# Performance work log

Hardware: AMD Instinct MI355X
Metric: run time of the kernel (lower is better)

## Reference

```python
import jax, jax.numpy as jnp
import numpy as np

NH = 12      # attention heads
EPS = 1e-5   # torch nn.LayerNorm default


def _ln(x, g, b):
    m = jnp.mean(x, axis=-1, keepdims=True)
    v = jnp.var(x, axis=-1, keepdims=True)
    return (x - m) * jax.lax.rsqrt(v + EPS) * g + b


def _rel_table(table, n):
    # q_size == k_size == n, table length == 2n-1 -> pure gather, no interpolation
    idx = jnp.arange(n)[:, None] - jnp.arange(n)[None, :] + (n - 1)
    return table[idx]  # (n, n, head_dim)


def _attn2d(x, qkv_w, qkv_b, proj_w, proj_b, rel_h, rel_w):
    B, H, W, C = x.shape
    hd = C // NH
    scale = hd ** -0.5
    N = H * W
    qkv = x.reshape(B, N, C) @ qkv_w + qkv_b                    # (B, N, 3C)
    qkv = qkv.reshape(B, N, 3, NH, hd).transpose(2, 0, 3, 1, 4).reshape(3, B * NH, N, hd)
    q, k, v = qkv[0], qkv[1], qkv[2]
    attn = jnp.einsum('bnd,bmd->bnm', q * scale, k)             # (B*NH, N, N)
    Rh = _rel_table(rel_h, H)
    Rw = _rel_table(rel_w, W)
    rq = q.reshape(B * NH, H, W, hd)                            # unscaled q, as in torch
    bias_h = jnp.einsum('bhwc,hkc->bhwk', rq, Rh)
    bias_w = jnp.einsum('bhwc,wkc->bhwk', rq, Rw)
    attn = (attn.reshape(B * NH, H, W, H, W)
            + bias_h[:, :, :, :, None]
            + bias_w[:, :, :, None, :]).reshape(B * NH, N, N)
    attn = jax.nn.softmax(attn, axis=-1)
    out = (attn @ v).reshape(B, NH, H, W, hd).transpose(0, 2, 3, 1, 4).reshape(B, H, W, C)
    return out @ proj_w + proj_b


def _win_part(x, ws):
    B, H, W, C = x.shape
    ph = (ws - H % ws) % ws
    pw = (ws - W % ws) % ws
    x = jnp.pad(x, ((0, 0), (0, ph), (0, pw), (0, 0)))
    Hp, Wp = H + ph, W + pw
    x = x.reshape(B, Hp // ws, ws, Wp // ws, ws, C).transpose(0, 1, 3, 2, 4, 5)
    return x.reshape(-1, ws, ws, C), (Hp, Wp)


def _win_unpart(wins, ws, pad_hw, hw):
    Hp, Wp = pad_hw
    H, W = hw
    B = wins.shape[0] // (Hp * Wp // ws // ws)
    x = wins.reshape(B, Hp // ws, Wp // ws, ws, ws, -1).transpose(0, 1, 3, 2, 4, 5)
    x = x.reshape(B, Hp, Wp, -1)
    return x[:, :H, :W, :]


def _block(x, ws, ln1g, ln1b, qkvw, qkvb, projw, projb, relh, relw,
           ln2g, ln2b, mw1, mb1, mw2, mb2):
    shortcut = x
    x = _ln(x, ln1g, ln1b)
    if ws > 0:
        H, W = x.shape[1], x.shape[2]
        x, pad_hw = _win_part(x, ws)
    x = _attn2d(x, qkvw, qkvb, projw, projb, relh, relw)
    if ws > 0:
        x = _win_unpart(x, ws, pad_hw, (H, W))
    x = shortcut + x
    h = _ln(x, ln2g, ln2b)
    h = jax.nn.gelu(h @ mw1 + mb1, approximate=False) @ mw2 + mb2
    return x + h


def setup_inputs() -> dict:
    key = jax.random.key(0)
    def rnd(i, shape, s=0.02):
        return jax.random.normal(jax.random.fold_in(key, i), shape, jnp.float32) * s
    C, M, HD = 768, 3072, 64
    d = {
        'x': rnd(0, (1, 3, 1024, 1024), 1.0),
        'patch_w': rnd(1, (16, 16, 3, C)),
        'patch_b': rnd(2, (C,)),
        'pos_embed': rnd(3, (1, 64, 64, C)),
    }
    i = 4
    for s, L in (('1', 27), ('2', 127)):
        for name, shape in (('ln1g', (C,)), ('ln1b', (C,)), ('qkvw', (C, 3 * C)),
                            ('qkvb', (3 * C,)), ('projw', (C, C)), ('projb', (C,)),
                            ('relh', (L, HD)), ('relw', (L, HD)),
                            ('ln2g', (C,)), ('ln2b', (C,)),
                            ('mw1', (C, M)), ('mb1', (M,)), ('mw2', (M, C)), ('mb2', (C,))):
            d[name + s] = rnd(i, shape)
            i += 1
    for s in ('1', '2'):
        d['ln1g' + s] = d['ln1g' + s] + 1.0
        d['ln2g' + s] = d['ln2g' + s] + 1.0
    return d


def reference(x, patch_w, patch_b, pos_embed,
              ln1g1, ln1b1, qkvw1, qkvb1, projw1, projb1, relh1, relw1,
              ln2g1, ln2b1, mw11, mb11, mw21, mb21,
              ln1g2, ln1b2, qkvw2, qkvb2, projw2, projb2, relh2, relw2,
              ln2g2, ln2b2, mw12, mb12, mw22, mb22):
    # patch embed: 16x16 stride-16 conv, output NHWC (B, 64, 64, 768)
    feat = jax.lax.conv_general_dilated(
        x, patch_w, window_strides=(16, 16), padding='VALID',
        dimension_numbers=('NCHW', 'HWIO', 'NHWC'))
    feat = feat + patch_b + pos_embed
    feat = _block(feat, 14, ln1g1, ln1b1, qkvw1, qkvb1, projw1, projb1,
                  relh1, relw1, ln2g1, ln2b1, mw11, mb11, mw21, mb21)
    feat = _block(feat, 0, ln1g2, ln1b2, qkvw2, qkvb2, projw2, projb2,
                  relh2, relw2, ln2g2, ln2b2, mw12, mb12, mw22, mb22)
    return feat
```

## Files before the change

kernel.cpp:

```cpp
#include <hip/hip_runtime.h>


using u16 = unsigned short;
using u32 = unsigned int;
using short8  = __attribute__((ext_vector_type(8))) short;
using floatx4 = __attribute__((ext_vector_type(4))) float;

__device__ __forceinline__ float bfu2f(u16 u) { return __builtin_bit_cast(float, (u32)u << 16); }
__device__ __forceinline__ u16   f2bfu(float f) {
  u32 u = __builtin_bit_cast(u32, f);
  return (u16)((u + 0x7fffu + ((u >> 16) & 1u)) >> 16);
}
__device__ __forceinline__ u32 cvtpk_bf16(float a, float b) {
  u32 r; asm("v_cvt_pk_bf16_f32 %0, %1, %2" : "=v"(r) : "v"(a), "v"(b)); return r;
}
#define DIV14(x) (((x) * 4682) >> 16)
#define WAIT_VM0()   __builtin_amdgcn_s_waitcnt(0x3f70)
#define WAIT_LGKM0() __builtin_amdgcn_s_waitcnt(0xc07f)

__device__ __forceinline__ void gld_lds16(const u16* g, u16* l) {
  __builtin_amdgcn_global_load_lds(
      (const __attribute__((address_space(1))) u32*)g,
      (__attribute__((address_space(3))) u32*)l, 16, 0, 0);
}

__global__ __launch_bounds__(256) void detect_k(const u16* __restrict__ x, int* __restrict__ flag)
{
  __shared__ int tot;
  if (threadIdx.x == 0) tot = 0;
  __syncthreads();
  int cnt = 0;
  for (int i = threadIdx.x; i < 4096; i += 256) {
    int e = (x[2 * i] >> 7) & 0xFF;
    cnt += (e >= 100 && e <= 134) ? 1 : 0;
  }
  atomicAdd(&tot, cnt);
  __syncthreads();
  if (threadIdx.x == 0) *flag = (tot >= 2458) ? 1 : 0;
}

struct CvtEnt { const void* src; int n; int dstoff; };
struct CvtArgs { CvtEnt e[24]; int cnt; };

__global__ __launch_bounds__(256) void tobf_multi_k(CvtArgs a, u16* __restrict__ dst,
                                                    const int* __restrict__ flag)
{
  int gid = blockIdx.x * 256 + threadIdx.x;
  bool isbf = (*flag != 0);
  for (int t = 0; t < a.cnt; ++t)
    if (gid < a.e[t].n)
      dst[a.e[t].dstoff + gid] = isbf ? ((const u16*)a.e[t].src)[gid]
                                      : f2bfu(((const float*)a.e[t].src)[gid]);
}

__global__ __launch_bounds__(256) void tobf4_k(const void* __restrict__ src, u16* __restrict__ dst,
                                               int n4, const int* __restrict__ flag)
{
  int i = blockIdx.x * 256 + threadIdx.x;
  if (i >= n4) return;
  ushort4 o;
  if (*flag) o = ((const ushort4*)src)[i];
  else {
    float4 f = ((const float4*)src)[i];
    o.x = f2bfu(f.x); o.y = f2bfu(f.y); o.z = f2bfu(f.z); o.w = f2bfu(f.w);
  }
  ((ushort4*)dst)[i] = o;
}

struct TJob { const void* src; int dstoff; int K; int N; int blk0; };
struct TArgs { TJob j[6]; int njobs; };

__global__ __launch_bounds__(256) void tobfT_multi_k(TArgs a, u16* __restrict__ wa,
                                                     const int* __restrict__ flag)
{
  __shared__ u16 t[64][65];
  const int bid = blockIdx.x;
  int ji = 0;
  #pragma unroll
  for (int q = 1; q < 6; ++q) if (q < a.njobs && bid >= a.j[q].blk0) ji = q;
  const void* src = a.j[ji].src;
  u16* dst = wa + a.j[ji].dstoff;
  const int K = a.j[ji].K, N = a.j[ji].N;
  const int local = bid - a.j[ji].blk0;
  const int nx = N >> 6;
  const int bx = local % nx, by = local / nx;
  const int n0 = bx * 64, k0 = by * 64;
  const int r = threadIdx.x >> 2, c = (threadIdx.x & 3) * 16;
  if (*flag) {
    const u16* s = (const u16*)src + (size_t)(k0 + r) * N + n0 + c;
    union { uint4 v[2]; u16 e[16]; } u;
    u.v[0] = *(const uint4*)s; u.v[1] = *(const uint4*)(s + 8);
    #pragma unroll
    for (int j = 0; j < 16; ++j) t[c + j][r] = u.e[j];
  } else {
    const float* s = (const float*)src + (size_t)(k0 + r) * N + n0 + c;
    #pragma unroll
    for (int j = 0; j < 16; ++j) t[c + j][r] = f2bfu(s[j]);
  }
  __syncthreads();
  union { uint4 v[2]; u16 e[16]; } o;
  #pragma unroll
  for (int j = 0; j < 16; ++j) o.e[j] = t[r][c + j];
  u16* d = dst + (size_t)(n0 + r) * K + k0 + c;
  *(uint4*)d = o.v[0]; *(uint4*)(d + 8) = o.v[1];
}

__global__ __launch_bounds__(256) void im2col_k(const void* __restrict__ xv, u16* __restrict__ a,
                                                const int* __restrict__ flag)
{
  int t = blockIdx.x, tid = threadIdx.x;
  int py = t >> 6, px = t & 63;
  int ky = tid >> 4, kx = tid & 15;
  size_t src = (size_t)(py * 16 + ky) * 1024 + px * 16 + kx;
  u16 v0, v1, v2;
  if (*flag) {
    const u16* x = (const u16*)xv;
    v0 = x[src]; v1 = x[src + 1048576]; v2 = x[src + 2097152];
  } else {
    const float* x = (const float*)xv;
    v0 = f2bfu(x[src]); v1 = f2bfu(x[src + 1048576]); v2 = f2bfu(x[src + 2097152]);
  }
  size_t dst = (size_t)t * 768 + tid * 3;
  a[dst] = v0; a[dst + 1] = v1; a[dst + 2] = v2;
}

__global__ __launch_bounds__(256) void ln_k(const float* __restrict__ x,
                                            const u16* __restrict__ g,
                                            const u16* __restrict__ b,
                                            u16* __restrict__ y)
{
  const int t = blockIdx.x, tid = threadIdx.x;
  const float* xp = x + (size_t)t * 768;
  float v0 = xp[tid], v1 = xp[tid + 256], v2 = xp[tid + 512];
  float s = v0 + v1 + v2;
  float q = v0 * v0 + v1 * v1 + v2 * v2;
  #pragma unroll
  for (int off = 32; off; off >>= 1) { s += __shfl_xor(s, off); q += __shfl_xor(q, off); }
  __shared__ float red[8];
  int wid = tid >> 6, lane = tid & 63;
  if (lane == 0) { red[wid] = s; red[4 + wid] = q; }
  __syncthreads();
  s = red[0] + red[1] + red[2] + red[3];
  q = red[4] + red[5] + red[6] + red[7];
  float mean = s * (1.f / 768.f);
  float var  = q * (1.f / 768.f) - mean * mean;
  float rstd = rsqrtf(var + 1e-5f);
  u16* yp = y + (size_t)t * 768;
  yp[tid]       = f2bfu((v0 - mean) * rstd * bfu2f(g[tid])       + bfu2f(b[tid]));
  yp[tid + 256] = f2bfu((v1 - mean) * rstd * bfu2f(g[tid + 256]) + bfu2f(b[tid + 256]));
  yp[tid + 512] = f2bfu((v2 - mean) * rstd * bfu2f(g[tid + 512]) + bfu2f(b[tid + 512]));
}

__global__ __launch_bounds__(256) void ln_win_k(const float* __restrict__ x,
                                                const u16* __restrict__ g,
                                                const u16* __restrict__ b,
                                                u16* __restrict__ wout)
{
  const int t = blockIdx.x, tid = threadIdx.x;
  const int win = t / 196, tok = t - win * 196;
  const int ty = DIV14(tok), tx = tok - 14 * ty;
  const int gy = (win / 5) * 14 + ty, gx = (win % 5) * 14 + tx;
  u16* yp = wout + (size_t)t * 768;
  if (gy >= 64 || gx >= 64) {
    yp[tid] = 0; yp[tid + 256] = 0; yp[tid + 512] = 0;
    return;
  }
  const float* xp = x + (size_t)(gy * 64 + gx) * 768;
  float v0 = xp[tid], v1 = xp[tid + 256], v2 = xp[tid + 512];
  float s = v0 + v1 + v2;
  float q = v0 * v0 + v1 * v1 + v2 * v2;
  #pragma unroll
  for (int off = 32; off; off >>= 1) { s += __shfl_xor(s, off); q += __shfl_xor(q, off); }
  __shared__ float red[8];
  int wid = tid >> 6, lane = tid & 63;
  if (lane == 0) { red[wid] = s; red[4 + wid] = q; }
  __syncthreads();
  s = red[0] + red[1] + red[2] + red[3];
  q = red[4] + red[5] + red[6] + red[7];
  float mean = s * (1.f / 768.f);
  float var  = q * (1.f / 768.f) - mean * mean;
  float rstd = rsqrtf(var + 1e-5f);
  yp[tid]       = f2bfu((v0 - mean) * rstd * bfu2f(g[tid])       + bfu2f(b[tid]));
  yp[tid + 256] = f2bfu((v1 - mean) * rstd * bfu2f(g[tid + 256]) + bfu2f(b[tid + 256]));
  yp[tid + 512] = f2bfu((v2 - mean) * rstd * bfu2f(g[tid + 512]) + bfu2f(b[tid + 512]));
}

enum { MODE_FEAT = 0, MODE_QKV = 1, MODE_RES = 2, MODE_GELU = 3, MODE_OUT = 4 };

template<int BN>
__global__ __launch_bounds__(256) void mgemm_k(
    const u16* __restrict__ A, const u16* __restrict__ Bt, const u16* __restrict__ bias,
    int M, int N, int K, int mode,
    float* __restrict__ outf, u16* __restrict__ outb,
    const float* __restrict__ res, const u16* __restrict__ pos,
    u16* __restrict__ qb, u16* __restrict__ kb, u16* __restrict__ vt, int TW,
    const int* __restrict__ flagp)
{
  constexpr int NWN = BN / 64, NWM = 4 / NWN;
  constexpr int WTM = 128 / NWM;
  constexpr int MS = WTM / 16, NS = 4;
  __shared__ __align__(16) u16 As[2][128 * 32];
  __shared__ __align__(16) u16 Bs[2][BN * 32];
  const int tid = threadIdx.x;
  const int wid = tid >> 6, lane = tid & 63;
  const int l15 = lane & 15, quad = lane >> 4;
  const int wm = wid / NWN, wn = wid % NWN;
  const int m0 = blockIdx.y * 128, n0 = blockIdx.x * BN;

  floatx4 acc[MS][NS];
  #pragma unroll
  for (int i = 0; i < MS; ++i)
    #pragma unroll
    for (int j = 0; j < NS; ++j) acc[i][j] = (floatx4){0.f, 0.f, 0.f, 0.f};

  const int sr = lane >> 2, sc = (lane & 3) * 8;
  const u16* ag0 = A + (size_t)min(m0 + wid * 32 + sr,      M - 1) * K + sc;
  const u16* ag1 = A + (size_t)min(m0 + wid * 32 + 16 + sr, M - 1) * K + sc;
  const u16 *bg0 = nullptr, *bg1 = nullptr;
  if constexpr (BN == 128) {
    bg0 = Bt + (size_t)(n0 + wid * 32 + sr) * K + sc;
    bg1 = Bt + (size_t)(n0 + wid * 32 + 16 + sr) * K + sc;
  } else {
    bg0 = Bt + (size_t)(n0 + wid * 16 + sr) * K + sc;
  }

  auto issue = [&](int buf, int k0) {
    gld_lds16(ag0 + k0, &As[buf][(wid * 32) * 32]);
    gld_lds16(ag1 + k0, &As[buf][(wid * 32 + 16) * 32]);
    if constexpr (BN == 128) {
      gld_lds16(bg0 + k0, &Bs[buf][(wid * 32) * 32]);
      gld_lds16(bg1 + k0, &Bs[buf][(wid * 32 + 16) * 32]);
    } else {
      gld_lds16(bg0 + k0, &Bs[buf][(wid * 16) * 32]);
    }
  };

  issue(0, 0);
  int bufi = 0;
  for (int k0 = 0; k0 < K; k0 += 32, bufi ^= 1) {
    WAIT_VM0();
    __syncthreads();
    if (k0 + 32 < K) issue(bufi ^ 1, k0 + 32);
    short8 af[MS], bf[NS];
    #pragma unroll
    for (int ms = 0; ms < MS; ++ms)
      af[ms] = *(const short8*)&As[bufi][(wm * WTM + ms * 16 + l15) * 32 + quad * 8];
    #pragma unroll
    for (int ns = 0; ns < NS; ++ns)
      bf[ns] = *(const short8*)&Bs[bufi][(wn * 64 + ns * 16 + l15) * 32 + quad * 8];
    #pragma unroll
    for (int ms = 0; ms < MS; ++ms)
      #pragma unroll
      for (int ns = 0; ns < NS; ++ns)
        acc[ms][ns] = __builtin_amdgcn_mfma_f32_16x16x32_bf16(af[ms], bf[ns], acc[ms][ns], 0, 0, 0);
  }

  const bool outbf = (mode == MODE_OUT) ? (*flagp != 0) : false;
  #pragma unroll
  for (int ms = 0; ms < MS; ++ms) {
    const int gmb = m0 + wm * WTM + ms * 16 + quad * 4;
    #pragma unroll
    for (int ns = 0; ns < NS; ++ns) {
      const int gn = n0 + wn * 64 + ns * 16 + l15;
      const float bb = bfu2f(bias[gn]);
      if (mode == MODE_QKV) {
        const int s = gn / 768, nn = gn - s * 768, h = nn >> 6, d = nn & 63;
        #pragma unroll
        for (int r = 0; r < 4; ++r) {
          int gm = gmb + r; if (gm >= M) continue;
          float v = acc[ms][ns][r] + bb;
          int b = gm / TW, tok = gm - b * TW;
          size_t bh = (size_t)(b * 12 + h);
          if (s == 0)      qb[(bh * TW + tok) * 64 + d] = f2bfu(v);
          else if (s == 1) kb[(bh * TW + tok) * 64 + d] = f2bfu(v);
          else             vt[(bh * 64 + d) * TW + tok] = f2bfu(v);
        }
      } else {
        #pragma unroll
        for (int r = 0; r < 4; ++r) {
          int gm = gmb + r; if (gm >= M) continue;
          size_t o = (size_t)gm * N + gn;
          float v = acc[ms][ns][r] + bb;
          if (mode == MODE_FEAT)      outf[o] = v + bfu2f(pos[o]);
          else if (mode == MODE_RES)  outf[o] = v + res[o];
          else if (mode == MODE_GELU) outb[o] = f2bfu(0.5f * v * (1.f + erff(v * 0.70710678f)));
          else {
            float ov = v + res[o];
            if (outbf) outb[o] = f2bfu(ov);
            else       outf[o] = ov;
          }
        }
      }
    }
  }
}

template<int NT, int TD, bool WIN>
__global__ __launch_bounds__(256) void flash_k(
    const u16* __restrict__ qb, const u16* __restrict__ kb, const u16* __restrict__ vt,
    const u16* __restrict__ relh, const u16* __restrict__ relw,
    u16* __restrict__ outb)
{
  constexpr int NTAB = 2 * TD - 1;
  constexpr int KT = (NT + 63) >> 6;
  constexpr float L2E = 1.4426950408889634f;
  constexpr float SC2 = 0.125f * L2E;
  constexpr int RQ  = 0;
  constexpr int RK0 = 4096;
  constexpr int RK1 = WIN ? 4096 : 8192;
  constexpr int RV0 = WIN ? 8192 : 12288;
  constexpr int RV1 = WIN ? 8192 : 16384;
  constexpr int RG  = WIN ? 12288 : 20480;
  constexpr int GWWIN = RG + 64 * 34;
  constexpr int TOT = WIN ? (GWWIN + 64 * 34) : (RG + 64 * 66);
  __shared__ __align__(16) u16 lds[TOT];

  const int tid = threadIdx.x, wid = tid >> 6, lane = tid & 63;
  const int l15 = lane & 15, quad = lane >> 4;
  const int qt = blockIdx.x, bh = blockIdx.y;
  const int q0 = qt * 64;
  const size_t kvbase = (size_t)bh * NT * 64;
  const size_t vbase  = (size_t)bh * 64 * NT;
  const int myrow = wid * 16 + l15;

  auto swb = [](int row, int blk) { return row * 64 + (((blk ^ row) & 7) << 3); };

  {
    const int r = tid >> 2, cb = (tid & 3) * 2;
    const int tok = min(q0 + r, NT - 1);
    const uint4* p = (const uint4*)(qb + kvbase + (size_t)tok * 64 + cb * 8);
    *(uint4*)&lds[RQ + swb(r, cb)]     = p[0];
    *(uint4*)&lds[RQ + swb(r, cb + 1)] = p[1];
  }
  __syncthreads();
  short8 qf[2];
  qf[0] = *(const short8*)&lds[RQ + swb(myrow, quad)];
  qf[1] = *(const short8*)&lds[RQ + swb(myrow, 4 + quad)];
  WAIT_LGKM0();

  auto stageRB = [&](const u16* tab, int rowoff, int maxrow) {
    const int r = tid >> 2, cb = (tid & 3) * 2;
    const int tr = min(rowoff + r, maxrow);
    const uint4* p = (const uint4*)(tab + (size_t)tr * 64 + cb * 8);
    *(uint4*)&lds[RV0 + swb(r, cb)]     = p[0];
    *(uint4*)&lds[RV0 + swb(r, cb + 1)] = p[1];
  };
  auto gpass = [&](int gbase, int gstride, int ncols) {
    for (int ns = 0; ns < ncols / 16; ++ns) {
      floatx4 g = (floatx4){0.f, 0.f, 0.f, 0.f};
      #pragma unroll
      for (int ks = 0; ks < 2; ++ks) {
        short8 b = *(const short8*)&lds[RV0 + swb(ns * 16 + l15, ks * 4 + quad)];
        g = __builtin_amdgcn_mfma_f32_16x16x32_bf16(qf[ks], b, g, 0, 0, 0);
      }
      #pragma unroll
      for (int r = 0; r < 4; ++r)
        lds[gbase + (wid * 16 + quad * 4 + r) * gstride + ns * 16 + l15] = f2bfu(g[r] * L2E);
    }
  };

  float gwv[4][4];
  if constexpr (!WIN) {
    stageRB(relh, qt, NTAB - 1);  __syncthreads();
    gpass(RG, 66, 64);
    __syncthreads();
    stageRB(relw, 0, NTAB - 1);   __syncthreads();
    gpass(RK0, 66, 64);
    #pragma unroll
    for (int kbi = 0; kbi < 4; ++kbi)
      #pragma unroll
      for (int r = 0; r < 4; ++r) {
        const int iw = myrow + 63 - (kbi * 16 + quad * 4 + r);
        if (iw < 64) gwv[kbi][r] = bfu2f(lds[RK0 + myrow * 66 + iw]);
      }
    WAIT_LGKM0();
    __syncthreads();
    stageRB(relw, 64, NTAB - 1);  __syncthreads();
    gpass(RK0, 66, 64);
    #pragma unroll
    for (int kbi = 0; kbi < 4; ++kbi)
      #pragma unroll
      for (int r = 0; r < 4; ++r) {
        const int iw = myrow + 63 - (kbi * 16 + quad * 4 + r);
        if (iw >= 64) gwv[kbi][r] = bfu2f(lds[RK0 + myrow * 66 + iw - 64]);
      }
    WAIT_LGKM0();
  } else {
    stageRB(relh, 0, NTAB - 1);  __syncthreads();
    gpass(RG, 34, 32);
    __syncthreads();
    stageRB(relw, 0, NTAB - 1);  __syncthreads();
    gpass(GWWIN, 34, 32);
  }

  const int srow = lane >> 3;
  const int scol = (((lane & 7) ^ srow) & 7) << 3;
  const u16* kp  = kb + kvbase + (size_t)(wid * 16 + srow) * 64 + scol;
  const u16* kp2 = kp + 512;
  const u16* vp  = vt + vbase  + (size_t)(wid * 16 + srow) * NT + scol;
  const u16* vp2 = vp + (size_t)8 * NT;
  u16* const kd0 = &lds[RK0 + wid * 1024];
  u16* const kd1 = &lds[RK1 + wid * 1024];
  u16* const vd0 = &lds[RV0 + wid * 1024];
  u16* const vd1 = &lds[RV1 + wid * 1024];
  auto issueKV = [&](int buf) {
    u16* kdb = buf ? kd1 : kd0;
    u16* vdb = buf ? vd1 : vd0;
    gld_lds16(kp,  kdb);
    gld_lds16(kp2, kdb + 512);
    gld_lds16(vp,  vdb);
    gld_lds16(vp2, vdb + 512);
    kp += 4096; kp2 += 4096; vp += 64; vp2 += 64;
  };

  float mI = -3e38f, lI = 0.f;
  floatx4 Oacc[4];
  #pragma unroll
  for (int d = 0; d < 4; ++d) Oacc[d] = (floatx4){0.f, 0.f, 0.f, 0.f};

  int qy = 0, qx = 0;
  if constexpr (WIN) {
    const int tok0 = q0 + myrow;
    qy = DIV14(tok0); qx = tok0 - 14 * qy;
  }

  auto body = [&](int RKb, int RVb, int kt) {
    floatx4 sacc[4];
    #pragma unroll
    for (int kbi = 0; kbi < 4; ++kbi) sacc[kbi] = (floatx4){0.f, 0.f, 0.f, 0.f};
    __builtin_amdgcn_s_setprio(1);
    #pragma unroll
    for (int ks = 0; ks < 2; ++ks)
      #pragma unroll
      for (int kbi = 0; kbi < 4; ++kbi) {
        short8 a = *(const short8*)&lds[RKb + swb(kbi * 16 + l15, ks * 4 + quad)];
        sacc[kbi] = __builtin_amdgcn_mfma_f32_16x16x32_bf16(a, qf[ks], sacc[kbi], 0, 0, 0);
      }
    __builtin_amdgcn_s_setprio(0);

    float sv[4][4];
    if constexpr (!WIN) {
      #pragma unroll
      for (int kbi = 0; kbi < 4; ++kbi)
        #pragma unroll
        for (int r = 0; r < 4; ++r)
          sv[kbi][r] = fmaf(SC2, sacc[kbi][r], gwv[kbi][r]);
    } else {
      #pragma unroll
      for (int kbi = 0; kbi < 4; ++kbi)
        #pragma unroll
        for (int r = 0; r < 4; ++r) {
          const int j = kt * 64 + kbi * 16 + quad * 4 + r;
          const int ky = DIV14(j), kx = j - 14 * ky;
          int ih = qy - ky + 13; ih = max(0, min(ih, 31));
          int iw = qx - kx + 13; iw = max(0, min(iw, 31));
          float s = SC2 * sacc[kbi][r] + bfu2f(lds[RG + myrow * 34 + ih])
                                       + bfu2f(lds[GWWIN + myrow * 34 + iw]);
          sv[kbi][r] = (j < NT) ? s : -1e30f;
        }
    }

    float rm;
    {
      float a0 = fmaxf(fmaxf(sv[0][0], sv[0][1]), fmaxf(sv[0][2], sv[0][3]));
      float a1 = fmaxf(fmaxf(sv[1][0], sv[1][1]), fmaxf(sv[1][2], sv[1][3]));
      float a2 = fmaxf(fmaxf(sv[2][0], sv[2][1]), fmaxf(sv[2][2], sv[2][3]));
      float a3 = fmaxf(fmaxf(sv[3][0], sv[3][1]), fmaxf(sv[3][2], sv[3][3]));
      rm = fmaxf(fmaxf(a0, a1), fmaxf(a2, a3));
    }
    rm = fmaxf(rm, __shfl_xor(rm, 16));
    rm = fmaxf(rm, __shfl_xor(rm, 32));
    float ghv = 0.f;
    if constexpr (!WIN) ghv = bfu2f(lds[RG + myrow * 66 + (63 - kt)]);
    const float mt = rm + ghv;
    const float mn = fmaxf(mI, mt);
    const float tt = mn - ghv;

    float rs = 0.f;
    u32 pk[8];
    #pragma unroll
    for (int kbi = 0; kbi < 4; ++kbi) {
      float p0 = __builtin_amdgcn_exp2f(sv[kbi][0] - tt);
      float p1 = __builtin_amdgcn_exp2f(sv[kbi][1] - tt);
      float p2 = __builtin_amdgcn_exp2f(sv[kbi][2] - tt);
      float p3 = __builtin_amdgcn_exp2f(sv[kbi][3] - tt);
      rs += (p0 + p1) + (p2 + p3);
      pk[2 * kbi]     = cvtpk_bf16(p0, p1);
      pk[2 * kbi + 1] = cvtpk_bf16(p2, p3);
    }

    #pragma unroll
    for (int kbi = 0; kbi < 4; ++kbi) {
      const int col = kbi * 16 + quad * 4;
      uint2 w2; w2.x = pk[2 * kbi]; w2.y = pk[2 * kbi + 1];
      *(uint2*)&lds[RQ + myrow * 64 + ((((col >> 3) ^ myrow) & 7) << 3) + (col & 7)] = w2;
    }

    const float al = __builtin_amdgcn_exp2f(mI - mn);
    if (__any(mt > mI)) {
      #pragma unroll
      for (int d = 0; d < 4; ++d) Oacc[d] *= al;
    }
    mI = mn;

    __builtin_amdgcn_s_setprio(1);
    #pragma unroll
    for (int ks = 0; ks < 2; ++ks) {
      short8 pb = *(const short8*)&lds[RQ + swb(myrow, ks * 4 + quad)];
      #pragma unroll
      for (int d = 0; d < 4; ++d) {
        short8 a = *(const short8*)&lds[RVb + swb(d * 16 + l15, ks * 4 + quad)];
        Oacc[d] = __builtin_amdgcn_mfma_f32_16x16x32_bf16(a, pb, Oacc[d], 0, 0, 0);
      }
    }
    __builtin_amdgcn_s_setprio(0);

    rs += __shfl_xor(rs, 16);
    rs += __shfl_xor(rs, 32);
    lI = fmaf(lI, al, rs);
  };

  if constexpr (!WIN) {
    __syncthreads();
    issueKV(0);
    for (int kt = 0; kt < KT; kt += 2) {
      WAIT_VM0();
      __syncthreads();
      if (kt + 1 < KT) issueKV(1);
      body(RK0, RV0, kt);
      WAIT_VM0();
      __syncthreads();
      if (kt + 2 < KT) issueKV(0);
      body(RK1, RV1, kt + 1);
    }
  } else {
    for (int kt = 0; kt < KT; ++kt) {
      __syncthreads();
      {
        const int r = tid >> 2, cb = (tid & 3) * 2;
        const int key = min(kt * 64 + r, NT - 1);
        const uint4* p = (const uint4*)(kb + kvbase + (size_t)key * 64 + cb * 8);
        *(uint4*)&lds[RK0 + swb(r, cb)]     = p[0];
        *(uint4*)&lds[RK0 + swb(r, cb + 1)] = p[1];
      }
      {
        const int d = tid >> 2, c = (tid & 3) << 4;
        if (kt * 64 + c + 15 < NT) {
          #pragma unroll
          for (int h = 0; h < 4; ++h) {
            uint2 v = *(const uint2*)(vt + vbase + (size_t)d * NT + kt * 64 + c + h * 4);
            const int col = c + h * 4;
            *(uint2*)&lds[RV0 + d * 64 + ((((col >> 3) ^ d) & 7) << 3) + (col & 7)] = v;
          }
        } else {
          #pragma unroll
          for (int j = 0; j < 16; ++j) {
            int key = min(kt * 64 + c + j, NT - 1);
            const int col = c + j;
            lds[RV0 + d * 64 + ((((col >> 3) ^ d) & 7) << 3) + (col & 7)] =
                vt[vbase + (size_t)d * NT + key];
          }
        }
      }
      __syncthreads();
      body(RK0, RV0, kt);
    }
  }

  const float rinv = 1.f / lI;
  const int tok = q0 + myrow;
  u32 ow[8];
  #pragma unroll
  for (int d = 0; d < 4; ++d) {
    ow[2 * d]     = cvtpk_bf16(Oacc[d][0] * rinv, Oacc[d][1] * rinv);
    ow[2 * d + 1] = cvtpk_bf16(Oacc[d][2] * rinv, Oacc[d][3] * rinv);
  }
  if constexpr (WIN) {
    if (tok < NT) {
      const int win = bh / 12, h = bh - win * 12;
      const int ty = DIV14(tok), tx = tok - 14 * ty;
      const int gy = (win / 5) * 14 + ty, gx = (win % 5) * 14 + tx;
      if (gy < 64 && gx < 64) {
        u16* op = outb + (size_t)(gy * 64 + gx) * 768 + h * 64;
        #pragma unroll
        for (int d = 0; d < 4; ++d)
          *(uint2*)(op + d * 16 + quad * 4) = make_uint2(ow[2 * d], ow[2 * d + 1]);
      }
    }
  } else {
    u16* op = outb + (size_t)tok * 768 + bh * 64;
    #pragma unroll
    for (int d = 0; d < 4; ++d)
      *(uint2*)(op + d * 16 + quad * 4) = make_uint2(ow[2 * d], ow[2 * d + 1]);
  }
}

extern "C" void kernel_launch(void* const* d_in, const int* in_sizes, int n_in,
                              void* d_out, int out_size, void* d_ws, size_t ws_size,
                              hipStream_t stream)
{
  const void* x      = d_in[0];
  const void* patchw = d_in[1];
  const void* patchb = d_in[2];
  const void* pos    = d_in[3];
  const void *ln1g1 = d_in[4],  *ln1b1 = d_in[5];
  const void *qkvw1 = d_in[6],  *qkvb1 = d_in[7];
  const void *projw1= d_in[8],  *projb1= d_in[9];
  const void *relh1 = d_in[10], *relw1 = d_in[11];
  const void *ln2g1 = d_in[12], *ln2b1 = d_in[13];
  const void *mw11  = d_in[14], *mb11  = d_in[15];
  const void *mw21  = d_in[16], *mb21  = d_in[17];
  const void *ln1g2 = d_in[18], *ln1b2 = d_in[19];
  const void *qkvw2 = d_in[20], *qkvb2 = d_in[21];
  const void *projw2= d_in[22], *projb2= d_in[23];
  const void *relh2 = d_in[24], *relw2 = d_in[25];
  const void *ln2g2 = d_in[26], *ln2b2 = d_in[27];
  const void *mw12  = d_in[28], *mb12  = d_in[29];
  const void *mw22  = d_in[30], *mb22  = d_in[31];

  char* w = (char*)d_ws;
  int*   FLAG = (int*)w;  w += 64;
  float* R0 = (float*)w;  w += 12582912;
  float* R1 = (float*)w;  w += 12582912;
  u16*   B0 = (u16*)w;    w += 6291456;
  u16*   Wb = (u16*)w;    w += 7526400;
  u16*   QB = (u16*)w;    w += 7526400;
  u16*   KB = (u16*)w;    w += 7526400;
  u16*   VT = (u16*)w;    w += 7526400;
  u16*   Hb = (u16*)w;    w += 25165824;
  u16*   WA = (u16*)w;    w += 15335424;
  u16*   POSb = (u16*)w;  w += 6291456;
  u16*   PRM = (u16*)w;   w += 106560;
  u16*   Ap = Hb;

  constexpr int WA_QKV = 0, WA_PROJ = 1769472, WA_M1 = 2359296, WA_M2 = 4718592,
                WA_PATCH = 7077888;
  constexpr int PRM_PATCHB = 0, PB1 = 768, PBLK = 26240, PB2 = 768 + PBLK;
  constexpr int O_QKVB = 0, O_PROJB = 2304, O_MB1 = 3072, O_MB2 = 6144,
                O_LN1G = 6912, O_LN1B = 7680, O_LN2G = 8448, O_LN2B = 9216,
                O_RELH = 9984, O_RELW = 18112;

  detect_k<<<1, 256, 0, stream>>>((const u16*)x, FLAG);
  CvtArgs ca; int kk = 0;
  auto add = [&](const void* s, int n, int off) { ca.e[kk].src = s; ca.e[kk].n = n; ca.e[kk].dstoff = off; ++kk; };
  add(patchb, 768, PRM_PATCHB);
  add(qkvb1, 2304, PB1 + O_QKVB); add(projb1, 768, PB1 + O_PROJB);
  add(mb11, 3072, PB1 + O_MB1);   add(mb21, 768, PB1 + O_MB2);
  add(ln1g1, 768, PB1 + O_LN1G);  add(ln1b1, 768, PB1 + O_LN1B);
  add(ln2g1, 768, PB1 + O_LN2G);  add(ln2b1, 768, PB1 + O_LN2B);
  add(relh1, 27 * 64, PB1 + O_RELH); add(relw1, 27 * 64, PB1 + O_RELW);
  add(qkvb2, 2304, PB2 + O_QKVB); add(projb2, 768, PB2 + O_PROJB);
  add(mb12, 3072, PB2 + O_MB1);   add(mb22, 768, PB2 + O_MB2);
  add(ln1g2, 768, PB2 + O_LN1G);  add(ln1b2, 768, PB2 + O_LN1B);
  add(ln2g2, 768, PB2 + O_LN2G);  add(ln2b2, 768, PB2 + O_LN2B);
  add(relh2, 127 * 64, PB2 + O_RELH); add(relw2, 127 * 64, PB2 + O_RELW);
  ca.cnt = kk;
  tobf_multi_k<<<32, 256, 0, stream>>>(ca, PRM, FLAG);
  tobf4_k<<<3072, 256, 0, stream>>>(pos, POSb, 786432, FLAG);

  {
    TArgs ta; int nb = 0, jn = 0;
    auto addT = [&](const void* s, int dstoff, int K, int N) {
      ta.j[jn] = { s, dstoff, K, N, nb }; nb += (N >> 6) * (K >> 6); ++jn;
    };
    addT(patchw, WA_PATCH, 768, 768);
    addT(qkvw1,  WA_QKV,   768, 2304);
    addT(projw1, WA_PROJ,  768, 768);
    addT(mw11,   WA_M1,    768, 3072);
    addT(mw21,   WA_M2,   3072, 768);
    ta.njobs = jn;
    tobfT_multi_k<<<nb, 256, 0, stream>>>(ta, WA, FLAG);
  }

  im2col_k<<<4096, 256, 0, stream>>>(x, Ap, FLAG);
  mgemm_k<64><<<dim3(12, 32), 256, 0, stream>>>(Ap, WA + WA_PATCH, PRM + PRM_PATCHB,
      4096, 768, 768, MODE_FEAT, R0, nullptr, nullptr, POSb, nullptr, nullptr, nullptr, 0, FLAG);

  ln_win_k<<<4900, 256, 0, stream>>>(R0, PRM + PB1 + O_LN1G, PRM + PB1 + O_LN1B, Wb);
  mgemm_k<128><<<dim3(18, 39), 256, 0, stream>>>(Wb, WA + WA_QKV, PRM + PB1 + O_QKVB,
      4900, 2304, 768, MODE_QKV, nullptr, nullptr, nullptr, nullptr, QB, KB, VT, 196, FLAG);
  flash_k<196, 14, true><<<dim3(4, 300), 256, 0, stream>>>(QB, KB, VT,
      PRM + PB1 + O_RELH, PRM + PB1 + O_RELW, B0);
  mgemm_k<64><<<dim3(12, 32), 256, 0, stream>>>(B0, WA + WA_PROJ, PRM + PB1 + O_PROJB,
      4096, 768, 768, MODE_RES, R1, nullptr, R0, nullptr, nullptr, nullptr, nullptr, 0, FLAG);
  ln_k<<<4096, 256, 0, stream>>>(R1, PRM + PB1 + O_LN2G, PRM + PB1 + O_LN2B, B0);
  mgemm_k<128><<<dim3(24, 32), 256, 0, stream>>>(B0, WA + WA_M1, PRM + PB1 + O_MB1,
      4096, 3072, 768, MODE_GELU, nullptr, Hb, nullptr, nullptr, nullptr, nullptr, nullptr, 0, FLAG);
  mgemm_k<64><<<dim3(12, 32), 256, 0, stream>>>(Hb, WA + WA_M2, PRM + PB1 + O_MB2,
      4096, 768, 3072, MODE_RES, R0, nullptr, R1, nullptr, nullptr, nullptr, nullptr, 0, FLAG);

  {
    TArgs ta; int nb = 0, jn = 0;
    auto addT = [&](const void* s, int dstoff, int K, int N) {
      ta.j[jn] = { s, dstoff, K, N, nb }; nb += (N >> 6) * (K >> 6); ++jn;
    };
    addT(qkvw2,  WA_QKV,  768, 2304);
    addT(projw2, WA_PROJ, 768, 768);
    addT(mw12,   WA_M1,   768, 3072);
    addT(mw22,   WA_M2,  3072, 768);
    ta.njobs = jn;
    tobfT_multi_k<<<nb, 256, 0, stream>>>(ta, WA, FLAG);
  }

  ln_k<<<4096, 256, 0, stream>>>(R0, PRM + PB2 + O_LN1G, PRM + PB2 + O_LN1B, B0);
  mgemm_k<128><<<dim3(18, 32), 256, 0, stream>>>(B0, WA + WA_QKV, PRM + PB2 + O_QKVB,
      4096, 2304, 768, MODE_QKV, nullptr, nullptr, nullptr, nullptr, QB, KB, VT, 4096, FLAG);
  flash_k<4096, 64, false><<<dim3(64, 12), 256, 0, stream>>>(QB, KB, VT,
      PRM + PB2 + O_RELH, PRM + PB2 + O_RELW, B0);
  mgemm_k<64><<<dim3(12, 32), 256, 0, stream>>>(B0, WA + WA_PROJ, PRM + PB2 + O_PROJB,
      4096, 768, 768, MODE_RES, R1, nullptr, R0, nullptr, nullptr, nullptr, nullptr, 0, FLAG);
  ln_k<<<4096, 256, 0, stream>>>(R1, PRM + PB2 + O_LN2G, PRM + PB2 + O_LN2B, B0);
  mgemm_k<128><<<dim3(24, 32), 256, 0, stream>>>(B0, WA + WA_M1, PRM + PB2 + O_MB1,
      4096, 3072, 768, MODE_GELU, nullptr, Hb, nullptr, nullptr, nullptr, nullptr, nullptr, 0, FLAG);
  mgemm_k<64><<<dim3(12, 32), 256, 0, stream>>>(Hb, WA + WA_M2, PRM + PB2 + O_MB2,
      4096, 768, 3072, MODE_OUT, (float*)d_out, (u16*)d_out, R1, nullptr, nullptr, nullptr, nullptr, 0, FLAG);
}
```

Baseline: 778.6 us.

## Split-K the narrow GEMMs with atomics and pad windowed attention to 256 tokens

The N=768 GEMMs (patch embed, attention projection, MLP down) now run with a split-K of 2 over gridDim.z. Partial sums are accumulated with float atomics into zero-filled buffers, and only slice 0 adds bias, residual or position terms. This doubles the block count on a 384-block grid to fill more CUs, at the cost of memsets, atomic traffic and a separate output conversion kernel. Separately, the windowed Q/K/V layout is padded from 196 to 256 tokens per window, with V pre-zeroed. This lets the windowed flash path reuse the double-buffered async KV pipeline instead of its synchronous scalar-fallback load loop.

Result: no change. 788.8 us (+1.3%).

```diff
diff --git a/kernel.cpp b/kernel.cpp
--- a/kernel.cpp
+++ b/kernel.cpp
@@ -65,6 +65,21 @@
     o.x = f2bfu(f.x); o.y = f2bfu(f.y); o.z = f2bfu(f.z); o.w = f2bfu(f.w);
   }
   ((ushort4*)dst)[i] = o;
+}
+
+__global__ __launch_bounds__(256) void cvt_out_k(const float* __restrict__ src,
+                                                 void* __restrict__ dst,
+                                                 const int* __restrict__ flag)
+{
+  int i = blockIdx.x * 256 + threadIdx.x;
+  float4 v = ((const float4*)src)[i];
+  if (*flag) {
+    ushort4 o;
+    o.x = f2bfu(v.x); o.y = f2bfu(v.y); o.z = f2bfu(v.z); o.w = f2bfu(v.w);
+    ((ushort4*)dst)[i] = o;
+  } else {
+    ((float4*)dst)[i] = v;
+  }
 }
 
 struct TJob { const void* src; int dstoff; int K; int N; int blk0; };
@@ -185,7 +200,7 @@
   yp[tid + 512] = f2bfu((v2 - mean) * rstd * bfu2f(g[tid + 512]) + bfu2f(b[tid + 512]));
 }
 
-enum { MODE_FEAT = 0, MODE_QKV = 1, MODE_RES = 2, MODE_GELU = 3, MODE_OUT = 4 };
+enum { MODE_QKV = 1, MODE_GELU = 3, MODE_FEATA = 5, MODE_RESA = 6 };
 
 template<int BN>
 __global__ __launch_bounds__(256) void mgemm_k(
@@ -193,7 +208,7 @@
     int M, int N, int K, int mode,
     float* __restrict__ outf, u16* __restrict__ outb,
     const float* __restrict__ res, const u16* __restrict__ pos,
-    u16* __restrict__ qb, u16* __restrict__ kb, u16* __restrict__ vt, int TW,
+    u16* __restrict__ qb, u16* __restrict__ kb, u16* __restrict__ vt, int TW, int TP,
     const int* __restrict__ flagp)
 {
   constexpr int NWN = BN / 64, NWM = 4 / NWN;
@@ -206,6 +221,10 @@
   const int l15 = lane & 15, quad = lane >> 4;
   const int wm = wid / NWN, wn = wid % NWN;
   const int m0 = blockIdx.y * 128, n0 = blockIdx.x * BN;
+  const int nz = (int)gridDim.z;
+  const int kloc = K / nz;
+  const int kbeg = blockIdx.z * kloc, kend = kbeg + kloc;
+  const bool z0 = (blockIdx.z == 0);
 
   floatx4 acc[MS][NS];
   #pragma unroll
@@ -235,12 +254,12 @@
     }
   };
 
-  issue(0, 0);
+  issue(0, kbeg);
   int bufi = 0;
-  for (int k0 = 0; k0 < K; k0 += 32, bufi ^= 1) {
+  for (int k0 = kbeg; k0 < kend; k0 += 32, bufi ^= 1) {
     WAIT_VM0();
     __syncthreads();
-    if (k0 + 32 < K) issue(bufi ^ 1, k0 + 32);
+    if (k0 + 32 < kend) issue(bufi ^ 1, k0 + 32);
     short8 af[MS], bf[NS];
     #pragma unroll
     for (int ms = 0; ms < MS; ++ms)
@@ -255,7 +274,6 @@
         acc[ms][ns] = __builtin_amdgcn_mfma_f32_16x16x32_bf16(af[ms], bf[ns], acc[ms][ns], 0, 0, 0);
   }
 
-  const bool outbf = (mode == MODE_OUT) ? (*flagp != 0) : false;
   #pragma unroll
   for (int ms = 0; ms < MS; ++ms) {
     const int gmb = m0 + wm * WTM + ms * 16 + quad * 4;
@@ -271,46 +289,57 @@
           float v = acc[ms][ns][r] + bb;
           int b = gm / TW, tok = gm - b * TW;
           size_t bh = (size_t)(b * 12 + h);
-          if (s == 0)      qb[(bh * TW + tok) * 64 + d] = f2bfu(v);
-          else if (s == 1) kb[(bh * TW + tok) * 64 + d] = f2bfu(v);
-          else             vt[(bh * 64 + d) * TW + tok] = f2bfu(v);
+          if (s == 0)      qb[(bh * TP + tok) * 64 + d] = f2bfu(v);
+          else if (s == 1) kb[(bh * TP + tok) * 64 + d] = f2bfu(v);
+          else             vt[(bh * 64 + d) * TP + tok] = f2bfu(v);
+        }
+      } else if (mode == MODE_GELU) {
+        #pragma unroll
+        for (int r = 0; r < 4; ++r) {
+          int gm = gmb + r; if (gm >= M) continue;
+          size_t o = (size_t)gm * N + gn;
+          float v = acc[ms][ns][r] + bb;
+          outb[o] = f2bfu(0.5f * v * (1.f + erff(v * 0.70710678f)));
+        }
+      } else if (mode == MODE_FEATA) {
+        #pragma unroll
+        for (int r = 0; r < 4; ++r) {
+          int gm = gmb + r; if (gm >= M) continue;
+          size_t o = (size_t)gm * N + gn;
+          float v = acc[ms][ns][r];
+          if (z0) v += bb + bfu2f(pos[o]);
+          unsafeAtomicAdd(&outf[o], v);
         }
       } else {
         #pragma unroll
         for (int r = 0; r < 4; ++r) {
           int gm = gmb + r; if (gm >= M) continue;
           size_t o = (size_t)gm * N + gn;
-          float v = acc[ms][ns][r] + bb;
-          if (mode == MODE_FEAT)      outf[o] = v + bfu2f(pos[o]);
-          else if (mode == MODE_RES)  outf[o] = v + res[o];
-          else if (mode == MODE_GELU) outb[o] = f2bfu(0.5f * v * (1.f + erff(v * 0.70710678f)));
-          else {
-            float ov = v + res[o];
-            if (outbf) outb[o] = f2bfu(ov);
-            else       outf[o] = ov;
-          }
+          float v = acc[ms][ns][r];
+          if (z0) v += bb + res[o];
+          unsafeAtomicAdd(&outf[o], v);
         }
       }
     }
   }
 }
 
-template<int NT, int TD, bool WIN>
+template<int NT, int NTP, int TD, bool WIN>
 __global__ __launch_bounds__(256) void flash_k(
     const u16* __restrict__ qb, const u16* __restrict__ kb, const u16* __restrict__ vt,
     const u16* __restrict__ relh, const u16* __restrict__ relw,
     u16* __restrict__ outb)
 {
   constexpr int NTAB = 2 * TD - 1;
-  constexpr int KT = (NT + 63) >> 6;
+  constexpr int KT = NTP >> 6;
   constexpr float L2E = 1.4426950408889634f;
   constexpr float SC2 = 0.125f * L2E;
   constexpr int RQ  = 0;
   constexpr int RK0 = 4096;
-  constexpr int RK1 = WIN ? 4096 : 8192;
-  constexpr int RV0 = WIN ? 8192 : 12288;
-  constexpr int RV1 = WIN ? 8192 : 16384;
-  constexpr int RG  = WIN ? 12288 : 20480;
+  constexpr int RK1 = 8192;
+  constexpr int RV0 = 12288;
+  constexpr int RV1 = 16384;
+  constexpr int RG  = 20480;
   constexpr int GWWIN = RG + 64 * 34;
   constexpr int TOT = WIN ? (GWWIN + 64 * 34) : (RG + 64 * 66);
   __shared__ __align__(16) u16 lds[TOT];
@@ -319,15 +348,15 @@
   const int l15 = lane & 15, quad = lane >> 4;
   const int qt = blockIdx.x, bh = blockIdx.y;
   const int q0 = qt * 64;
-  const size_t kvbase = (size_t)bh * NT * 64;
-  const size_t vbase  = (size_t)bh * 64 * NT;
+  const size_t kvbase = (size_t)bh * NTP * 64;
+  const size_t vbase  = (size_t)bh * 64 * NTP;
   const int myrow = wid * 16 + l15;
 
   auto swb = [](int row, int blk) { return row * 64 + (((blk ^ row) & 7) << 3); };
 
   {
     const int r = tid >> 2, cb = (tid & 3) * 2;
-    const int tok = min(q0 + r, NT - 1);
+    const int tok = WIN ? (q0 + r) : min(q0 + r, NT - 1);
     const uint4* p = (const uint4*)(qb + kvbase + (size_t)tok * 64 + cb * 8);
     *(uint4*)&lds[RQ + swb(r, cb)]     = p[0];
     *(uint4*)&lds[RQ + swb(r, cb + 1)] = p[1];
@@ -397,8 +426,8 @@
   const int scol = (((lane & 7) ^ srow) & 7) << 3;
   const u16* kp  = kb + kvbase + (size_t)(wid * 16 + srow) * 64 + scol;
   const u16* kp2 = kp + 512;
-  const u16* vp  = vt + vbase  + (size_t)(wid * 16 + srow) * NT + scol;
-  const u16* vp2 = vp + (size_t)8 * NT;
+  const u16* vp  = vt + vbase  + (size_t)(wid * 16 + srow) * NTP + scol;
+  const u16* vp2 = vp + (size_t)8 * NTP;
   u16* const kd0 = &lds[RK0 + wid * 1024];
   u16* const kd1 = &lds[RK1 + wid * 1024];
   u16* const vd0 = &lds[RV0 + wid * 1024];
@@ -520,51 +549,17 @@
     lI = fmaf(lI, al, rs);
   };
 
-  if constexpr (!WIN) {
+  __syncthreads();
+  issueKV(0);
+  for (int kt = 0; kt < KT; kt += 2) {
+    WAIT_VM0();
     __syncthreads();
-    issueKV(0);
-    for (int kt = 0; kt < KT; kt += 2) {
-      WAIT_VM0();
-      __syncthreads();
-      if (kt + 1 < KT) issueKV(1);
-      body(RK0, RV0, kt);
-      WAIT_VM0();
-      __syncthreads();
-      if (kt + 2 < KT) issueKV(0);
-      body(RK1, RV1, kt + 1);
-    }
-  } else {
-    for (int kt = 0; kt < KT; ++kt) {
-      __syncthreads();
-      {
-        const int r = tid >> 2, cb = (tid & 3) * 2;
-        const int key = min(kt * 64 + r, NT - 1);
-        const uint4* p = (const uint4*)(kb + kvbase + (size_t)key * 64 + cb * 8);
-        *(uint4*)&lds[RK0 + swb(r, cb)]     = p[0];
-        *(uint4*)&lds[RK0 + swb(r, cb + 1)] = p[1];
-      }
-      {
-        const int d = tid >> 2, c = (tid & 3) << 4;
-        if (kt * 64 + c + 15 < NT) {
-          #pragma unroll
-          for (int h = 0; h < 4; ++h) {
-            uint2 v = *(const uint2*)(vt + vbase + (size_t)d * NT + kt * 64 + c + h * 4);
-            const int col = c + h * 4;
-            *(uint2*)&lds[RV0 + d * 64 + ((((col >> 3) ^ d) & 7) << 3) + (col & 7)] = v;
-          }
-        } else {
-          #pragma unroll
-          for (int j = 0; j < 16; ++j) {
-            int key = min(kt * 64 + c + j, NT - 1);
-            const int col = c + j;
-            lds[RV0 + d * 64 + ((((col >> 3) ^ d) & 7) << 3) + (col & 7)] =
-                vt[vbase + (size_t)d * NT + key];
-          }
-        }
-      }
-      __syncthreads();
-      body(RK0, RV0, kt);
-    }
+    if (kt + 1 < KT) issueKV(1);
+    body(RK0, RV0, kt);
+    WAIT_VM0();
+    __syncthreads();
+    if (kt + 2 < KT) issueKV(0);
+    body(RK1, RV1, kt + 1);
   }
 
   const float rinv = 1.f / lI;
@@ -624,9 +619,9 @@
   float* R1 = (float*)w;  w += 12582912;
   u16*   B0 = (u16*)w;    w += 6291456;
   u16*   Wb = (u16*)w;    w += 7526400;
-  u16*   QB = (u16*)w;    w += 7526400;
-  u16*   KB = (u16*)w;    w += 7526400;
-  u16*   VT = (u16*)w;    w += 7526400;
+  u16*   QB = (u16*)w;    w += 9830400;
+  u16*   KB = (u16*)w;    w += 9830400;
+  u16*   VT = (u16*)w;    w += 9830400;
   u16*   Hb = (u16*)w;    w += 25165824;
   u16*   WA = (u16*)w;    w += 15335424;
   u16*   POSb = (u16*)w;  w += 6291456;
@@ -673,21 +668,25 @@
   }
 
   im2col_k<<<4096, 256, 0, stream>>>(x, Ap, FLAG);
-  mgemm_k<64><<<dim3(12, 32), 256, 0, stream>>>(Ap, WA + WA_PATCH, PRM + PRM_PATCHB,
-      4096, 768, 768, MODE_FEAT, R0, nullptr, nullptr, POSb, nullptr, nullptr, nullptr, 0, FLAG);
+  hipMemsetAsync(R0, 0, 12582912, stream);
+  mgemm_k<64><<<dim3(12, 32, 2), 256, 0, stream>>>(Ap, WA + WA_PATCH, PRM + PRM_PATCHB,
+      4096, 768, 768, MODE_FEATA, R0, nullptr, nullptr, POSb, nullptr, nullptr, nullptr, 0, 0, FLAG);
 
   ln_win_k<<<4900, 256, 0, stream>>>(R0, PRM + PB1 + O_LN1G, PRM + PB1 + O_LN1B, Wb);
+  hipMemsetAsync(VT, 0, 9830400, stream);
   mgemm_k<128><<<dim3(18, 39), 256, 0, stream>>>(Wb, WA + WA_QKV, PRM + PB1 + O_QKVB,
-      4900, 2304, 768, MODE_QKV, nullptr, nullptr, nullptr, nullptr, QB, KB, VT, 196, FLAG);
-  flash_k<196, 14, true><<<dim3(4, 300), 256, 0, stream>>>(QB, KB, VT,
+      4900, 2304, 768, MODE_QKV, nullptr, nullptr, nullptr, nullptr, QB, KB, VT, 196, 256, FLAG);
+  flash_k<196, 256, 14, true><<<dim3(4, 300), 256, 0, stream>>>(QB, KB, VT,
       PRM + PB1 + O_RELH, PRM + PB1 + O_RELW, B0);
-  mgemm_k<64><<<dim3(12, 32), 256, 0, stream>>>(B0, WA + WA_PROJ, PRM + PB1 + O_PROJB,
-      4096, 768, 768, MODE_RES, R1, nullptr, R0, nullptr, nullptr, nullptr, nullptr, 0, FLAG);
+  hipMemsetAsync(R1, 0, 12582912, stream);
+  mgemm_k<64><<<dim3(12, 32, 2), 256, 0, stream>>>(B0, WA + WA_PROJ, PRM + PB1 + O_PROJB,
+      4096, 768, 768, MODE_RESA, R1, nullptr, R0, nullptr, nullptr, nullptr, nullptr, 0, 0, FLAG);
   ln_k<<<4096, 256, 0, stream>>>(R1, PRM + PB1 + O_LN2G, PRM + PB1 + O_LN2B, B0);
   mgemm_k<128><<<dim3(24, 32), 256, 0, stream>>>(B0, WA + WA_M1, PRM + PB1 + O_MB1,
-      4096, 3072, 768, MODE_GELU, nullptr, Hb, nullptr, nullptr, nullptr, nullptr, nullptr, 0, FLAG);
-  mgemm_k<64><<<dim3(12, 32), 256, 0, stream>>>(Hb, WA + WA_M2, PRM + PB1 + O_MB2,
-      4096, 768, 3072, MODE_RES, R0, nullptr, R1, nullptr, nullptr, nullptr, nullptr, 0, FLAG);
+      4096, 3072, 768, MODE_GELU, nullptr, Hb, nullptr, nullptr, nullptr, nullptr, nullptr, 0, 0, FLAG);
+  hipMemsetAsync(R0, 0, 12582912, stream);
+  mgemm_k<64><<<dim3(12, 32, 2), 256, 0, stream>>>(Hb, WA + WA_M2, PRM + PB1 + O_MB2,
+      4096, 768, 3072, MODE_RESA, R0, nullptr, R1, nullptr, nullptr, nullptr, nullptr, 0, 0, FLAG);
 
   {
     TArgs ta; int nb = 0, jn = 0;
@@ -704,14 +703,17 @@
 
   ln_k<<<4096, 256, 0, stream>>>(R0, PRM + PB2 + O_LN1G, PRM + PB2 + O_LN1B, B0);
   mgemm_k<128><<<dim3(18, 32), 256, 0, stream>>>(B0, WA + WA_QKV, PRM + PB2 + O_QKVB,
-      4096, 2304, 768, MODE_QKV, nullptr, nullptr, nullptr, nullptr, QB, KB, VT, 4096, FLAG);
-  flash_k<4096, 64, false><<<dim3(64, 12), 256, 0, stream>>>(QB, KB, VT,
+      4096, 2304, 768, MODE_QKV, nullptr, nullptr, nullptr, nullptr, QB, KB, VT, 4096, 4096, FLAG);
+  flash_k<4096, 4096, 64, false><<<dim3(64, 12), 256, 0, stream>>>(QB, KB, VT,
       PRM + PB2 + O_RELH, PRM + PB2 + O_RELW, B0);
-  mgemm_k<64><<<dim3(12, 32), 256, 0, stream>>>(B0, WA + WA_PROJ, PRM + PB2 + O_PROJB,
-      4096, 768, 768, MODE_RES, R1, nullptr, R0, nullptr, nullptr, nullptr, nullptr, 0, FLAG);
+  hipMemsetAsync(R1, 0, 12582912, stream);
+  mgemm_k<64><<<dim3(12, 32, 2), 256, 0, stream>>>(B0, WA + WA_PROJ, PRM + PB2 + O_PROJB,
+      4096, 768, 768, MODE_RESA, R1, nullptr, R0, nullptr, nullptr, nullptr, nullptr, 0, 0, FLAG);
   ln_k<<<4096, 256, 0, stream>>>(R1, PRM + PB2 + O_LN2G, PRM + PB2 + O_LN2B, B0);
   mgemm_k<128><<<dim3(24, 32), 256, 0, stream>>>(B0, WA + WA_M1, PRM + PB2 + O_MB1,
-      4096, 3072, 768, MODE_GELU, nullptr, Hb, nullptr, nullptr, nullptr, nullptr, nullptr, 0, FLAG);
-  mgemm_k<64><<<dim3(12, 32), 256, 0, stream>>>(Hb, WA + WA_M2, PRM + PB2 + O_MB2,
-      4096, 768, 3072, MODE_OUT, (float*)d_out, (u16*)d_out, R1, nullptr, nullptr, nullptr, nullptr, 0, FLAG);
-}
+      4096, 3072, 768, MODE_GELU, nullptr, Hb, nullptr, nullptr, nullptr, nullptr, nullptr, 0, 0, FLAG);
+  hipMemsetAsync(R0, 0, 12582912, stream);
+  mgemm_k<64><<<dim3(12, 32, 2), 256, 0, stream>>>(Hb, WA + WA_M2, PRM + PB2 + O_MB2,
+      4096, 768, 3072, MODE_RESA, R0, nullptr, R1, nullptr, nullptr, nullptr, nullptr, 0, 0, FLAG);
+  cvt_out_k<<<3072, 256, 0, stream>>>(R0, d_out, FLAG);
+}
```
